# Performance work log

Measured on AMD Instinct MI355X. Metric: run time of the kernel, lower is better.

Reference implementation:

```python
import jax, jax.numpy as jnp
import numpy as np

EMBED_DIM = 1024
NUM_HEADS = 16
KEY_SIZE = 1024
VALUE_SIZE = 1024
N, L = 4, 2048


def setup_inputs() -> dict:
    key = jax.random.key(0)
    ks = jax.random.split(key, 8)
    s = lambda fan_in: 1.0 / np.sqrt(fan_in)
    return {
        "x": jax.random.normal(ks[0], (N, L, EMBED_DIM), dtype=jnp.float32),
        # nn.Linear weights stored as (out, in); we apply x @ W.T
        "W_q": jax.random.uniform(ks[1], (KEY_SIZE, EMBED_DIM), jnp.float32, -s(EMBED_DIM), s(EMBED_DIM)),
        "W_k": jax.random.uniform(ks[2], (KEY_SIZE, EMBED_DIM), jnp.float32, -s(EMBED_DIM), s(EMBED_DIM)),
        "W_v": jax.random.uniform(ks[3], (VALUE_SIZE, EMBED_DIM), jnp.float32, -s(EMBED_DIM), s(EMBED_DIM)),
        "W_qp": jax.random.uniform(ks[4], (KEY_SIZE, KEY_SIZE), jnp.float32, -s(KEY_SIZE), s(KEY_SIZE)),
        "W_kp": jax.random.uniform(ks[5], (KEY_SIZE, KEY_SIZE), jnp.float32, -s(KEY_SIZE), s(KEY_SIZE)),
        "W_vp": jax.random.uniform(ks[6], (VALUE_SIZE, VALUE_SIZE), jnp.float32, -s(VALUE_SIZE), s(VALUE_SIZE)),
        "W_out": jax.random.uniform(ks[7], (EMBED_DIM, VALUE_SIZE), jnp.float32, -s(VALUE_SIZE), s(VALUE_SIZE)),
    }


def reference(x, W_q, W_k, W_v, W_qp, W_kp, W_vp, W_out):
    H = NUM_HEADS
    q = (x @ W_q.T) @ W_qp.T   # (N, L, key_size)
    k = (x @ W_k.T) @ W_kp.T   # (N, L, key_size)
    v = (x @ W_v.T) @ W_vp.T   # (N, L, value_size)
    n, l, vs = v.shape
    dq = q.shape[-1] // H
    dv = vs // H
    q = q.reshape(n, l, H, dq).transpose(0, 2, 1, 3)  # (N, H, L, dq)
    k = k.reshape(n, l, H, dq).transpose(0, 2, 1, 3)
    v = v.reshape(n, l, H, dv).transpose(0, 2, 1, 3)
    att = jnp.einsum("nhid,nhjd->nhij", q, k) / jnp.sqrt(jnp.float32(dq))
    att = jax.nn.softmax(att, axis=-1)
    out = jnp.einsum("nhij,nhjd->nhid", att, v)       # (N, H, L, dv)
    out = out.transpose(0, 2, 1, 3).reshape(n, l, vs)
    return out @ W_out.T
```

## Files before the change

kernel.cpp:

```cpp
#include <hip/hip_runtime.h>
#include <cstddef>
#include <cstdint>

#define EMBED 1024
#define NH    16
#define DQ    64
#define NB    4
#define LSEQ  2048
#define MROWS (NB * LSEQ)

typedef __bf16 bf16x8 __attribute__((ext_vector_type(8)));
typedef __bf16 bf16x4 __attribute__((ext_vector_type(4)));
typedef float  f32x4  __attribute__((ext_vector_type(4)));

__device__ __forceinline__ unsigned short f2bf(float f) {
    return (unsigned short)((__float_as_uint(f) + 0x8000u) >> 16);
}

__device__ __forceinline__ unsigned pack2(float a, float b) {
    unsigned ua = __float_as_uint(a) + 0x8000u;
    unsigned ub = __float_as_uint(b) + 0x8000u;
    return __builtin_amdgcn_perm(ub, ua, 0x07060302u);
}

__device__ __forceinline__ uint2 pack4(float a, float b, float c, float d) {
    return make_uint2(pack2(a, b), pack2(c, d));
}

__device__ __forceinline__ unsigned pack2t(float a, float b) {
    return __builtin_amdgcn_perm(__float_as_uint(b), __float_as_uint(a), 0x07060302u);
}

__device__ __forceinline__ void async_cp16(const void* g, void* l) {
    __builtin_amdgcn_global_load_lds((const __attribute__((address_space(1))) unsigned int*)g,
                                     (__attribute__((address_space(3))) unsigned int*)l,
                                     16, 0, 0);
}

struct CvtJobs {
    const float* src[8];
    unsigned short* dst[8];
    int n[8];
};

__global__ __launch_bounds__(256) void cvt_bf16(CvtJobs j) {
    int job = blockIdx.y;
    const float* s = j.src[job];
    unsigned short* d = j.dst[job];
    int n4 = j.n[job] >> 2;
    int stride = gridDim.x * blockDim.x;
    for (int i = blockIdx.x * blockDim.x + threadIdx.x; i < n4; i += stride) {
        float4 f = ((const float4*)s)[i];
        ((uint2*)d)[i] = pack4(f.x, f.y, f.z, f.w);
    }
}

struct TransJobs {
    const float* src[3];
    unsigned short* dst[3];
};

__global__ __launch_bounds__(256) void transpose_cvt(TransJobs tj) {
    __shared__ unsigned short Ts[64][68];
    const float* src = tj.src[blockIdx.z];
    unsigned short* dst = tj.dst[blockIdx.z];
    const int tid = threadIdx.x;
    const int r0 = blockIdx.y * 64;
    const int c0 = blockIdx.x * 64;

    {
        int col4 = tid & 15;
        int rb   = tid >> 4;
#pragma unroll
        for (int it = 0; it < 4; it++) {
            int r = rb + it * 16;
            float4 f = *(const float4*)(src + (size_t)(r0 + r) * 1024 + c0 + col4 * 4);
            *(uint2*)&Ts[r][col4 * 4] = pack4(f.x, f.y, f.z, f.w);
        }
    }
    __syncthreads();

    {
        int oc = tid >> 2;
        int seg = tid & 3;
        __attribute__((aligned(16))) unsigned short tmp[16];
#pragma unroll
        for (int e = 0; e < 16; e++) tmp[e] = Ts[seg * 16 + e][oc];
        unsigned short* out = dst + (size_t)(c0 + oc) * 1024 + r0 + seg * 16;
        *(uint4*)(out)     = *(const uint4*)&tmp[0];
        *(uint4*)(out + 8) = *(const uint4*)&tmp[8];
    }
}

struct BGemmArgs {
    const unsigned short* A[3];
    const unsigned short* B[3];
    void* C[3];
    int mode[3];
    float scl[3];
};

__global__ __launch_bounds__(256) void gemm_bf16nt(BGemmArgs p, int M, int N, int K) {
    __shared__ __align__(16) unsigned short SMEM[2 * 128 * 64];
    unsigned short* As = SMEM;
    unsigned short* Bs = SMEM + 128 * 64;

    const int tid  = threadIdx.x;
    const int wave = tid >> 6;
    const int lane = tid & 63;
    const int m16  = lane & 15;
    const int kq   = lane >> 4;

    const int nwg  = gridDim.x * gridDim.y;
    const int flat = blockIdx.y * gridDim.x + blockIdx.x;
    const int swz  = (flat & 7) * (nwg >> 3) + (flat >> 3);
    const int bm = (swz / gridDim.x) * 128;
    const int bn = (swz % gridDim.x) * 128;
    const int z  = blockIdx.z;
    const unsigned short* A = p.A[z];
    const unsigned short* B = p.B[z];

    f32x4 acc[4][4];
#pragma unroll
    for (int i = 0; i < 4; i++)
#pragma unroll
        for (int j = 0; j < 4; j++) acc[i][j] = f32x4{0.f, 0.f, 0.f, 0.f};

    const int wr = (wave >> 1) * 64;
    const int wc = (wave & 1) * 64;

    for (int k0 = 0; k0 < K; k0 += 64) {
#pragma unroll
        for (int it = 0; it < 4; it++) {
            int c = tid + it * 256;
            int r = c >> 3;
            int kc = (c & 7) ^ (r & 7);
            async_cp16(A + (size_t)(bm + r) * K + k0 + kc * 8,
                       &As[(it * 256 + wave * 64) * 8]);
            async_cp16(B + (size_t)(bn + r) * K + k0 + kc * 8,
                       &Bs[(it * 256 + wave * 64) * 8]);
        }
        __syncthreads();

#pragma unroll
        for (int s = 0; s < 2; s++) {
            bf16x8 af[4], bfr[4];
#pragma unroll
            for (int i = 0; i < 4; i++) {
                int ra = wr + i * 16 + m16;
                af[i] = *reinterpret_cast<const bf16x8*>(
                    &As[ra * 64 + (((s * 4 + kq) ^ (ra & 7)) * 8)]);
                int rb = wc + i * 16 + m16;
                bfr[i] = *reinterpret_cast<const bf16x8*>(
                    &Bs[rb * 64 + (((s * 4 + kq) ^ (rb & 7)) * 8)]);
            }
#pragma unroll
            for (int i = 0; i < 4; i++)
#pragma unroll
                for (int j = 0; j < 4; j++)
                    acc[i][j] = __builtin_amdgcn_mfma_f32_16x16x32_bf16(af[i], bfr[j], acc[i][j], 0, 0, 0);
        }
        __syncthreads();
    }

    const int mode = p.mode[z];
    const float scl = p.scl[z];
    if (mode == 0) {
        unsigned short* Cb = (unsigned short*)p.C[z];
#pragma unroll
        for (int i = 0; i < 4; i++)
#pragma unroll
            for (int j = 0; j < 4; j++) {
                int row = bm + wr + i * 16 + kq * 4;
                int col = bn + wc + j * 16 + m16;
#pragma unroll
                for (int q = 0; q < 4; q++)
                    Cb[(size_t)(row + q) * N + col] = f2bf(acc[i][j][q] * scl);
            }
    } else if (mode == 1) {
        float* Cf = (float*)p.C[z];
#pragma unroll
        for (int i = 0; i < 4; i++)
#pragma unroll
            for (int j = 0; j < 4; j++) {
                int row = bm + wr + i * 16 + kq * 4;
                int col = bn + wc + j * 16 + m16;
#pragma unroll
                for (int q = 0; q < 4; q++)
                    Cf[(size_t)(row + q) * N + col] = acc[i][j][q];
            }
    } else {
        unsigned short* Tt = SMEM;
#pragma unroll
        for (int i = 0; i < 4; i++)
#pragma unroll
            for (int j = 0; j < 4; j++) {
                int c = wc + j * 16 + m16;
                int u = (wr >> 2) + i * 4 + kq;
                int us = (u + 2 * c) & 31;
                *reinterpret_cast<uint2*>(&Tt[c * 128 + us * 4]) =
                    pack4(acc[i][j][0], acc[i][j][1], acc[i][j][2], acc[i][j][3]);
            }
        __syncthreads();
        unsigned short* Ct = (unsigned short*)p.C[z];
        int r8 = tid & 15;
        int cb = tid >> 4;
#pragma unroll
        for (int pass = 0; pass < 8; pass++) {
            int c  = pass * 16 + cb;
            int u0 = r8 * 2;
            int us = (u0 + 2 * c) & 31;
            uint4 val = *reinterpret_cast<const uint4*>(&Tt[c * 128 + us * 4]);
            *reinterpret_cast<uint4*>(&Ct[(size_t)(bn + c) * M + bm + r8 * 8]) = val;
        }
    }
}

__global__ __launch_bounds__(256, 4)
void flash_bf16(const unsigned short* __restrict__ qb,
                const unsigned short* __restrict__ kb,
                const unsigned short* __restrict__ vtb,
                unsigned short* __restrict__ ao) {
    __shared__ __align__(16) unsigned short Ks[2][64 * 64];
    __shared__ __align__(16) unsigned short Vt[2][64 * 64];

    const int tid  = threadIdx.x;
    const int wave = tid >> 6;
    const int lane = tid & 63;
    const int m16  = lane & 15;
    const int kq   = lane >> 4;

    const int flat = blockIdx.y * (LSEQ / 128) + blockIdx.x;
    const int swz  = (flat & 7) * 128 + (flat >> 3);
    const int bh   = swz >> 4;
    const int nn   = bh >> 4;
    const int h    = bh & 15;
    const int q0   = (swz & 15) * 128;

    const uint2 ones_u = make_uint2(0x3F803F80u, 0x3F803F80u);
    const bf16x4 ones4 = __builtin_bit_cast(bf16x4, ones_u);

    const unsigned short* kptr  = kb + (size_t)(nn * LSEQ) * EMBED + h * DQ;
    const unsigned short* vtptr = vtb + (size_t)(h * DQ) * MROWS + nn * LSEQ;

    auto stage = [&](int buf) {
#pragma unroll
        for (int it = 0; it < 2; it++) {
            int c = tid + it * 256;
            int r = c >> 3;
            int kc = (c & 7) ^ (r & 7);
            async_cp16(kptr + (size_t)r * EMBED + kc * 8,
                       &Ks[buf][(it * 256 + wave * 64) * 8]);
            async_cp16(vtptr + (size_t)r * MROWS + kc * 8,
                       &Vt[buf][(it * 256 + wave * 64) * 8]);
        }
        kptr  += 64 * EMBED;
        vtptr += 64;
    };

    stage(0);

    bf16x8 qf[2][2];
#pragma unroll
    for (int j = 0; j < 2; j++) {
        size_t tok = (size_t)(nn * LSEQ + q0 + wave * 32 + j * 16 + m16);
#pragma unroll
        for (int s = 0; s < 2; s++)
            qf[j][s] = *reinterpret_cast<const bf16x8*>(
                &qb[tok * EMBED + h * DQ + s * 32 + kq * 8]);
    }

    f32x4 o[4][2];
    f32x4 o4[2];
#pragma unroll
    for (int j = 0; j < 2; j++) {
        o4[j] = f32x4{0.f, 0.f, 0.f, 0.f};
#pragma unroll
        for (int mt = 0; mt < 4; mt++) o[mt][j] = f32x4{0.f, 0.f, 0.f, 0.f};
    }

    asm volatile("s_waitcnt vmcnt(0)" ::: "memory");
    __builtin_amdgcn_s_barrier();
    asm volatile("" ::: "memory");

    const int NT = LSEQ / 64;
    for (int kt = 0; kt < NT; kt++) {
        const int cur = kt & 1;
        if (kt + 1 < NT) stage(cur ^ 1);

        f32x4 st[4][2];
#pragma unroll
        for (int i = 0; i < 4; i++)
#pragma unroll
            for (int j = 0; j < 2; j++) st[i][j] = f32x4{0.f, 0.f, 0.f, 0.f};

#pragma unroll
        for (int s = 0; s < 2; s++) {
            bf16x8 ak[4];
#pragma unroll
            for (int i = 0; i < 4; i++) {
                int key = i * 16 + m16;
                ak[i] = *reinterpret_cast<const bf16x8*>(
                    &Ks[cur][key * 64 + (((s * 4 + kq) ^ (m16 & 7)) * 8)]);
            }
            __builtin_amdgcn_s_setprio(1);
#pragma unroll
            for (int i = 0; i < 4; i++)
#pragma unroll
                for (int j = 0; j < 2; j++)
                    st[i][j] = __builtin_amdgcn_mfma_f32_16x16x32_bf16(ak[i], qf[j][s], st[i][j], 0, 0, 0);
            __builtin_amdgcn_s_setprio(0);
        }

        bf16x4 pb[4][2];
#pragma unroll
        for (int i = 0; i < 4; i++)
#pragma unroll
            for (int j = 0; j < 2; j++) {
#pragma unroll
                for (int q = 0; q < 4; q++)
                    st[i][j][q] = __builtin_amdgcn_exp2f(st[i][j][q]);
                uint2 u = make_uint2(pack2t(st[i][j][0], st[i][j][1]),
                                     pack2t(st[i][j][2], st[i][j][3]));
                pb[i][j] = __builtin_bit_cast(bf16x4, u);
            }

#pragma unroll
        for (int i = 0; i < 4; i++) {
            bf16x4 av4[4];
#pragma unroll
            for (int mt = 0; mt < 4; mt++) {
                int d = mt * 16 + m16;
                av4[mt] = *reinterpret_cast<const bf16x4*>(
                    &Vt[cur][d * 64 + (((2 * i + (kq >> 1)) ^ (d & 7)) * 8) + (kq & 1) * 4]);
            }
            __builtin_amdgcn_s_setprio(1);
#pragma unroll
            for (int mt = 0; mt < 4; mt++)
#pragma unroll
                for (int j = 0; j < 2; j++)
                    o[mt][j] = __builtin_amdgcn_mfma_f32_16x16x16bf16_1k(av4[mt], pb[i][j], o[mt][j], 0, 0, 0);
#pragma unroll
            for (int j = 0; j < 2; j++)
                o4[j] = __builtin_amdgcn_mfma_f32_16x16x16bf16_1k(ones4, pb[i][j], o4[j], 0, 0, 0);
            __builtin_amdgcn_s_setprio(0);
        }

        if (kt + 1 < NT) {
            asm volatile("s_waitcnt vmcnt(0)" ::: "memory");
            __builtin_amdgcn_s_barrier();
            asm volatile("" ::: "memory");
        }
    }

#pragma unroll
    for (int j = 0; j < 2; j++) {
        float inv = 1.f / o4[j][0];
        size_t tok = (size_t)(nn * LSEQ + q0 + wave * 32 + j * 16 + m16);
#pragma unroll
        for (int mt = 0; mt < 4; mt++) {
            *reinterpret_cast<uint2*>(&ao[tok * EMBED + h * DQ + mt * 16 + kq * 4]) =
                pack4(o[mt][j][0] * inv, o[mt][j][1] * inv, o[mt][j][2] * inv, o[mt][j][3] * inv);
        }
    }
}

extern "C" void kernel_launch(void* const* d_in, const int* in_sizes, int n_in,
                              void* d_out, int out_size, void* d_ws, size_t ws_size,
                              hipStream_t stream) {
    (void)in_sizes; (void)n_in; (void)out_size; (void)ws_size;
    const float* x     = (const float*)d_in[0];
    const float* W_q   = (const float*)d_in[1];
    const float* W_k   = (const float*)d_in[2];
    const float* W_v   = (const float*)d_in[3];
    const float* W_qp  = (const float*)d_in[4];
    const float* W_kp  = (const float*)d_in[5];
    const float* W_vp  = (const float*)d_in[6];
    const float* W_out = (const float*)d_in[7];

    unsigned short* ws16 = (unsigned short*)d_ws;
    const size_t SZX = (size_t)MROWS * EMBED;
    const size_t SZW = (size_t)EMBED * EMBED;

    unsigned short* xb    = ws16;
    unsigned short* wqpb  = xb + SZX;
    unsigned short* wkpb  = wqpb + SZW;
    unsigned short* wvpb  = wkpb + SZW;
    unsigned short* woutb = wvpb + SZW;
    unsigned short* wqT   = woutb + SZW;
    unsigned short* wkT   = wqT + SZW;
    unsigned short* wvT   = wkT + SZW;
    unsigned short* weq   = wvT + SZW;
    unsigned short* wek   = weq + SZW;
    unsigned short* wev   = wek + SZW;
    unsigned short* qbuf  = wev + SZW;
    unsigned short* kbuf  = qbuf + SZX;
    unsigned short* vtbuf = kbuf + SZX;
    unsigned short* ao    = vtbuf + SZX;

    CvtJobs cj;
    cj.src[0] = x;     cj.dst[0] = xb;    cj.n[0] = (int)SZX;
    cj.src[1] = W_qp;  cj.dst[1] = wqpb;  cj.n[1] = (int)SZW;
    cj.src[2] = W_kp;  cj.dst[2] = wkpb;  cj.n[2] = (int)SZW;
    cj.src[3] = W_vp;  cj.dst[3] = wvpb;  cj.n[3] = (int)SZW;
    cj.src[4] = W_out; cj.dst[4] = woutb; cj.n[4] = (int)SZW;
    cvt_bf16<<<dim3(512, 5), 256, 0, stream>>>(cj);

    TransJobs tj;
    tj.src[0] = W_q; tj.src[1] = W_k; tj.src[2] = W_v;
    tj.dst[0] = wqT; tj.dst[1] = wkT; tj.dst[2] = wvT;
    transpose_cvt<<<dim3(16, 16, 3), 256, 0, stream>>>(tj);

    BGemmArgs fz;
    fz.A[0] = wqpb; fz.A[1] = wkpb; fz.A[2] = wvpb;
    fz.B[0] = wqT;  fz.B[1] = wkT;  fz.B[2] = wvT;
    fz.C[0] = weq;  fz.C[1] = wek;  fz.C[2] = wev;
    fz.mode[0] = 0; fz.mode[1] = 0; fz.mode[2] = 0;
    fz.scl[0] = 1.f; fz.scl[1] = 1.f; fz.scl[2] = 1.f;
    gemm_bf16nt<<<dim3(8, 8, 3), 256, 0, stream>>>(fz, EMBED, EMBED, EMBED);

    BGemmArgs pj;
    pj.A[0] = xb;   pj.A[1] = xb;   pj.A[2] = xb;
    pj.B[0] = weq;  pj.B[1] = wek;  pj.B[2] = wev;
    pj.C[0] = qbuf; pj.C[1] = kbuf; pj.C[2] = vtbuf;
    pj.mode[0] = 0; pj.mode[1] = 0; pj.mode[2] = 2;
    pj.scl[0] = 0.18033688f; pj.scl[1] = 1.f; pj.scl[2] = 1.f;
    gemm_bf16nt<<<dim3(8, 64, 3), 256, 0, stream>>>(pj, MROWS, EMBED, EMBED);

    flash_bf16<<<dim3(LSEQ / 128, NB * NH), 256, 0, stream>>>(qbuf, kbuf, vtbuf, ao);

    BGemmArgs og;
    og.A[0] = ao;    og.A[1] = ao;    og.A[2] = ao;
    og.B[0] = woutb; og.B[1] = woutb; og.B[2] = woutb;
    og.C[0] = d_out; og.C[1] = d_out; og.C[2] = d_out;
    og.mode[0] = 1; og.mode[1] = 1; og.mode[2] = 1;
    og.scl[0] = 1.f; og.scl[1] = 1.f; og.scl[2] = 1.f;
    gemm_bf16nt<<<dim3(8, 64, 1), 256, 0, stream>>>(og, MROWS, EMBED, EMBED);
}
```

Baseline: 305.8 us.

## Use 16x16x32 bf16 MFMA for PV by permuting V^T key layout in GEMM epilogue

The PV product and row-sum accumulation in the flash kernel now use the K=32 bf16 MFMA instead of K=16, halving the number of MFMA issues and V LDS reads per tile. To make the P fragment from two adjacent 16-key score tiles line up with an 8-wide V fragment, the projection GEMM epilogue writes V^T with keys permuted within each 32-key group. The exp2 and packing are interleaved per 32-key chunk. The risk is that the permuted layout must match exactly or results are wrong, and the epilogue now issues two 8-byte stores instead of one 16-byte store.

Measured after the change: 297.7 us. -2.7%, faster.

```diff
diff --git a/kernel.cpp b/kernel.cpp
--- a/kernel.cpp
+++ b/kernel.cpp
@@ -10,7 +10,6 @@
 #define MROWS (NB * LSEQ)
 
 typedef __bf16 bf16x8 __attribute__((ext_vector_type(8)));
-typedef __bf16 bf16x4 __attribute__((ext_vector_type(4)));
 typedef float  f32x4  __attribute__((ext_vector_type(4)));
 
 __device__ __forceinline__ unsigned short f2bf(float f) {
@@ -211,7 +210,12 @@
             int u0 = r8 * 2;
             int us = (u0 + 2 * c) & 31;
             uint4 val = *reinterpret_cast<const uint4*>(&Tt[c * 128 + us * 4]);
-            *reinterpret_cast<uint4*>(&Ct[(size_t)(bn + c) * M + bm + r8 * 8]) = val;
+            int key0 = r8 * 8;
+            int loc  = key0 & 31;
+            int dst0 = (key0 & 96) + (((loc & 15) >> 2) * 8) + ((loc >> 4) * 4);
+            unsigned short* out = &Ct[(size_t)(bn + c) * M + bm + dst0];
+            *reinterpret_cast<uint2*>(out)     = make_uint2(val.x, val.y);
+            *reinterpret_cast<uint2*>(out + 8) = make_uint2(val.z, val.w);
         }
     }
 }
@@ -237,8 +241,8 @@
     const int h    = bh & 15;
     const int q0   = (swz & 15) * 128;
 
-    const uint2 ones_u = make_uint2(0x3F803F80u, 0x3F803F80u);
-    const bf16x4 ones4 = __builtin_bit_cast(bf16x4, ones_u);
+    const uint4 ones_u = make_uint4(0x3F803F80u, 0x3F803F80u, 0x3F803F80u, 0x3F803F80u);
+    const bf16x8 ones8 = __builtin_bit_cast(bf16x8, ones_u);
 
     const unsigned short* kptr  = kb + (size_t)(nn * LSEQ) * EMBED + h * DQ;
     const unsigned short* vtptr = vtb + (size_t)(h * DQ) * MROWS + nn * LSEQ;
@@ -312,37 +316,41 @@
             __builtin_amdgcn_s_setprio(0);
         }
 
-        bf16x4 pb[4][2];
-#pragma unroll
-        for (int i = 0; i < 4; i++)
-#pragma unroll
-            for (int j = 0; j < 2; j++) {
-#pragma unroll
-                for (int q = 0; q < 4; q++)
-                    st[i][j][q] = __builtin_amdgcn_exp2f(st[i][j][q]);
-                uint2 u = make_uint2(pack2t(st[i][j][0], st[i][j][1]),
-                                     pack2t(st[i][j][2], st[i][j][3]));
-                pb[i][j] = __builtin_bit_cast(bf16x4, u);
-            }
-
-#pragma unroll
-        for (int i = 0; i < 4; i++) {
-            bf16x4 av4[4];
+#pragma unroll
+        for (int t = 0; t < 2; t++) {
+            bf16x8 av8[4];
 #pragma unroll
             for (int mt = 0; mt < 4; mt++) {
                 int d = mt * 16 + m16;
-                av4[mt] = *reinterpret_cast<const bf16x4*>(
-                    &Vt[cur][d * 64 + (((2 * i + (kq >> 1)) ^ (d & 7)) * 8) + (kq & 1) * 4]);
+                av8[mt] = *reinterpret_cast<const bf16x8*>(
+                    &Vt[cur][d * 64 + (((t * 4 + kq) ^ (m16 & 7)) * 8)]);
+            }
+#pragma unroll
+            for (int ii = 0; ii < 2; ii++)
+#pragma unroll
+                for (int j = 0; j < 2; j++)
+#pragma unroll
+                    for (int q = 0; q < 4; q++)
+                        st[2 * t + ii][j][q] = __builtin_amdgcn_exp2f(st[2 * t + ii][j][q]);
+            bf16x8 pb[2];
+#pragma unroll
+            for (int j = 0; j < 2; j++) {
+                uint4 pu;
+                pu.x = pack2t(st[2 * t][j][0],     st[2 * t][j][1]);
+                pu.y = pack2t(st[2 * t][j][2],     st[2 * t][j][3]);
+                pu.z = pack2t(st[2 * t + 1][j][0], st[2 * t + 1][j][1]);
+                pu.w = pack2t(st[2 * t + 1][j][2], st[2 * t + 1][j][3]);
+                pb[j] = __builtin_bit_cast(bf16x8, pu);
             }
             __builtin_amdgcn_s_setprio(1);
 #pragma unroll
             for (int mt = 0; mt < 4; mt++)
 #pragma unroll
                 for (int j = 0; j < 2; j++)
-                    o[mt][j] = __builtin_amdgcn_mfma_f32_16x16x16bf16_1k(av4[mt], pb[i][j], o[mt][j], 0, 0, 0);
+                    o[mt][j] = __builtin_amdgcn_mfma_f32_16x16x32_bf16(av8[mt], pb[j], o[mt][j], 0, 0, 0);
 #pragma unroll
             for (int j = 0; j < 2; j++)
-                o4[j] = __builtin_amdgcn_mfma_f32_16x16x16bf16_1k(ones4, pb[i][j], o4[j], 0, 0, 0);
+                o4[j] = __builtin_amdgcn_mfma_f32_16x16x32_bf16(ones8, pb[j], o4[j], 0, 0, 0);
             __builtin_amdgcn_s_setprio(0);
         }
 
```
